# Optimization experiments

Measured on AMD Instinct MI355X. Metric: run time of the kernel, lower is better.

## Reference

```python
import jax, jax.numpy as jnp
import numpy as np


def _skew_relative(QE):
    # QE: [B, H, N, 2N-1] -> [B, H, N, N] relative-position skew (Music-Transformer style)
    B, H, N, L = QE.shape  # L == 2N - 1
    x = jnp.pad(QE, ((0, 0), (0, 0), (0, 0), (0, 1))).reshape(B, H, N * (L + 1))
    x = jnp.pad(x, ((0, 0), (0, 0), (0, N - 1))).reshape(B, H, N + 1, 2 * N - 1)
    return x[:, :, :N, -N:]


def setup_inputs() -> dict:
    key = jax.random.key(0)
    ks = jax.random.split(key, 8)
    B, N, D, H, dh = 8, 1024, 512, 8, 64
    W_SCALE = 0.02
    return {
        "x": jax.random.normal(ks[0], (B, N, D), jnp.float32),
        "phase": jax.random.uniform(ks[1], (B, H, N, 1), jnp.float32),
        "E_rel": jax.random.normal(ks[2], (2 * N - 1, dh), jnp.float32) * 0.05,
        "W_q": jax.random.normal(ks[3], (H * dh, D), jnp.float32) * W_SCALE,
        "W_k": jax.random.normal(ks[4], (H * dh, D), jnp.float32) * W_SCALE,
        "W_v": jax.random.normal(ks[5], (H * dh, D), jnp.float32) * W_SCALE,
        "W_o": jax.random.normal(ks[6], (D, H * dh), jnp.float32) * W_SCALE,
        "b_o": jnp.zeros((D,), jnp.float32),
    }


def reference(x, phase, E_rel, W_q, W_k, W_v, W_o, b_o):
    B, N, _ = x.shape
    H = phase.shape[1]
    dh = W_q.shape[0] // H
    scale = 1.0 / (dh ** 0.5)

    def heads(W):  # [B,N,H*dh] -> [B,H,N,dh]
        return (x @ W.T).reshape(B, N, H, dh).transpose(0, 2, 1, 3)

    Q, K, V = heads(W_q), heads(W_k), heads(W_v)
    attn = jnp.einsum('bhnd,bhmd->bhnm', Q, K)
    attn = attn + _skew_relative(jnp.einsum('bhnd,ld->bhnl', Q, E_rel))
    attn = jax.nn.softmax(attn * scale, axis=-1)
    out = jnp.einsum('bhnm,bhmd->bhnd', attn, V) * phase  # phase-modulated AV
    out = out.transpose(0, 2, 1, 3).reshape(B, N, H * dh)
    return out @ W_o.T + b_o  # dropout is identity in eval mode
```

## Files before the change

### kernel.cpp

```cpp
#include <hip/hip_runtime.h>


typedef __bf16 bf16x8 __attribute__((ext_vector_type(8)));
typedef __bf16 bf16x4 __attribute__((ext_vector_type(4)));
typedef float  f32x4  __attribute__((ext_vector_type(4)));
typedef float  f32x16 __attribute__((ext_vector_type(16)));

#if __has_builtin(__builtin_amdgcn_exp2f)
#define EXP2(x) __builtin_amdgcn_exp2f(x)
#else
#define EXP2(x) exp2f(x)
#endif

#define QSCALE 0.18033688011f

#define GLOAD_LDS16(g, l)                                                      \
    __builtin_amdgcn_global_load_lds(                                          \
        (const __attribute__((address_space(1))) unsigned int*)(g),            \
        (__attribute__((address_space(3))) unsigned int*)(l), 16, 0, 0)


__global__ __launch_bounds__(256) void cvt_all(const float* __restrict__ x,
                                               const float* __restrict__ E,
                                               const float* __restrict__ wq,
                                               const float* __restrict__ wk,
                                               const float* __restrict__ wv,
                                               const float* __restrict__ wo,
                                               __bf16* __restrict__ xb,
                                               __bf16* __restrict__ Ef,
                                               __bf16* __restrict__ wqkv,
                                               __bf16* __restrict__ wob) {
    int i = blockIdx.x * 256 + threadIdx.x;
    if (i >= 1081328 ? i < 1343472 : i < 1048576) {
        const float* s; __bf16* d; int off;
        if      (i < 1048576) { s = x;  d = xb;            off = i; }
        else if (i < 1146864) { s = wq; d = wqkv;          off = i - 1081328; }
        else if (i < 1212400) { s = wk; d = wqkv + 262144; off = i - 1146864; }
        else if (i < 1277936) { s = wv; d = wqkv + 524288; off = i - 1212400; }
        else                  { s = wo; d = wob;           off = i - 1277936; }
        float4 v = *(const float4*)(s + (size_t)off * 4);
        bf16x4 o;
        o[0] = (__bf16)v.x; o[1] = (__bf16)v.y; o[2] = (__bf16)v.z; o[3] = (__bf16)v.w;
        *(bf16x4*)(d + (size_t)off * 4) = o;
    } else if (i >= 1048576 && i < 1081328) {
        int off = i - 1048576;
        float4 v = *(const float4*)(E + (size_t)off * 4);
        int e0i = off * 4;
        int l = e0i >> 6, d0 = e0i & 63;
        int t32 = l >> 5, cq = l & 31, ks = d0 >> 4, hf = (d0 >> 3) & 1, j = d0 & 7;
        bf16x4 o;
        o[0] = (__bf16)v.x; o[1] = (__bf16)v.y; o[2] = (__bf16)v.z; o[3] = (__bf16)v.w;
        *(bf16x4*)(Ef + ((size_t)((t32 * 4 + ks) * 64) + hf * 32 + cq) * 8 + j) = o;
    }
}

__global__ __launch_bounds__(256) void gemm_qkv(const __bf16* __restrict__ X,
                                                const __bf16* __restrict__ W,
                                                __bf16* __restrict__ Qb,
                                                __bf16* __restrict__ Kf,
                                                __bf16* __restrict__ Vf) {
    __shared__ __bf16 Xs[128][64];
    __shared__ __bf16 Ws[128][64];
    const int tid = threadIdx.x;
    const int wave = tid >> 6, lane = tid & 63;
    const int col = lane & 15, quad = lane >> 4;
    const int m_base = blockIdx.x * 128;
    const int j_base = blockIdx.y * 128;
    const bool qk = (j_base < 1024);
    const int wm = (wave & 1) * 64;
    const int wn = (wave >> 1) * 64;
    const f32x4 fz = {0.f, 0.f, 0.f, 0.f};
    f32x4 acc[4][4];
#pragma unroll
    for (int i = 0; i < 4; ++i)
#pragma unroll
        for (int j = 0; j < 4; ++j) acc[i][j] = fz;

    for (int k0 = 0; k0 < 512; k0 += 64) {
#pragma unroll
        for (int p = 0; p < 4; ++p) {
            int s = tid + p * 256;
            int row = s >> 3, cc = (s & 7) * 8;
            GLOAD_LDS16(X + (size_t)(m_base + row) * 512 + k0 + cc, &Xs[0][0] + (size_t)s * 8);
            GLOAD_LDS16(W + (size_t)(j_base + row) * 512 + k0 + cc, &Ws[0][0] + (size_t)s * 8);
        }
        __syncthreads();
#pragma unroll
        for (int kk = 0; kk < 64; kk += 32) {
            bf16x8 xa[4], wb[4];
#pragma unroll
            for (int i = 0; i < 4; ++i) xa[i] = *(const bf16x8*)(&Xs[wm + i * 16 + col][kk + quad * 8]);
#pragma unroll
            for (int j = 0; j < 4; ++j) wb[j] = *(const bf16x8*)(&Ws[wn + j * 16 + col][kk + quad * 8]);
            if (qk) {
#pragma unroll
                for (int i = 0; i < 4; ++i)
#pragma unroll
                    for (int j = 0; j < 4; ++j)
                        acc[i][j] = __builtin_amdgcn_mfma_f32_16x16x32_bf16(wb[i], xa[j], acc[i][j], 0, 0, 0);
            } else {
#pragma unroll
                for (int i = 0; i < 4; ++i)
#pragma unroll
                    for (int j = 0; j < 4; ++j)
                        acc[i][j] = __builtin_amdgcn_mfma_f32_16x16x32_bf16(xa[i], wb[j], acc[i][j], 0, 0, 0);
            }
        }
        __syncthreads();
    }
    if (qk) {
#pragma unroll
        for (int i = 0; i < 4; ++i) {
#pragma unroll
            for (int j = 0; j < 4; ++j) {
                int jabs = j_base + wn + i * 16 + quad * 4;
                int m = m_base + wm + j * 16 + col;
                int b_ = m >> 10, n = m & 1023;
                int rem = jabs & 511, h = rem >> 6, d = rem & 63;
                bf16x4 v;
                if (jabs < 512) {
                    v[0] = (__bf16)(acc[i][j][0] * QSCALE);
                    v[1] = (__bf16)(acc[i][j][1] * QSCALE);
                    v[2] = (__bf16)(acc[i][j][2] * QSCALE);
                    v[3] = (__bf16)(acc[i][j][3] * QSCALE);
                    *(bf16x4*)(Qb + (((size_t)b_ * 8 + h) * 1024 + n) * 64 + d) = v;
                } else {
                    v[0] = (__bf16)acc[i][j][0]; v[1] = (__bf16)acc[i][j][1];
                    v[2] = (__bf16)acc[i][j][2]; v[3] = (__bf16)acc[i][j][3];
                    int t32 = n >> 5, cq = n & 31, ks = d >> 4, hf = (d >> 3) & 1, jj = d & 7;
                    *(bf16x4*)(Kf + (size_t)(b_ * 8 + h) * 65536 +
                               ((size_t)((t32 * 4 + ks) * 64) + hf * 32 + cq) * 8 + jj) = v;
                }
            }
        }
    } else {
#pragma unroll
        for (int i = 0; i < 4; ++i) {
#pragma unroll
            for (int j = 0; j < 4; ++j) {
                int m = m_base + wm + i * 16 + quad * 4;
                int b_ = m >> 10, n = m & 1023;
                int jabs = j_base + wn + j * 16 + col;
                int rem = jabs & 511, h = rem >> 6, d = rem & 63;
                int t64 = n >> 6, ks = (n >> 4) & 3, hf = (n >> 3) & 1, jj = n & 7;
                int dhalf = d >> 5, cq = d & 31;
                bf16x4 v;
                v[0] = (__bf16)acc[i][j][0]; v[1] = (__bf16)acc[i][j][1];
                v[2] = (__bf16)acc[i][j][2]; v[3] = (__bf16)acc[i][j][3];
                *(bf16x4*)(Vf + (size_t)(b_ * 8 + h) * 65536 +
                           ((size_t)(((t64 * 4 + ks) * 2 + dhalf) * 64) + hf * 32 + cq) * 8 + jj) = v;
            }
        }
    }
}

__global__ __launch_bounds__(128, 2) void flash_kernel(const __bf16* __restrict__ Qb,
                                                       const __bf16* __restrict__ Kf,
                                                       const __bf16* __restrict__ Vf,
                                                       const __bf16* __restrict__ Ef,
                                                       const float* __restrict__ phase,
                                                       __bf16* __restrict__ Ob) {
    const int bid = blockIdx.x;
    const int bh = bid & 63;
    const int n0 = (bid >> 6) * 64;
    const int w = threadIdx.x >> 6, lane = threadIdx.x & 63;
    const int colq = lane & 31, half = lane >> 5;
    const int nbase = n0 + w * 32;

    __shared__ __bf16 Pw[2][32][72];

    f32x16 z16;
#pragma unroll
    for (int i = 0; i < 16; ++i) z16[i] = 0.f;

    bf16x8 a_q[4];
#pragma unroll
    for (int ks = 0; ks < 4; ++ks)
        a_q[ks] = *(const bf16x8*)(Qb + ((size_t)bh * 1024 + nbase + colq) * 64 + ks * 16 + half * 8);

    f32x16 o0 = z16, o1 = z16;
    float rowsum[16];
#pragma unroll
    for (int i = 0; i < 16; ++i) rowsum[i] = 0.f;

    const __bf16* Kfb = Kf + (size_t)bh * 65536;
    const __bf16* Vfb = Vf + (size_t)bh * 65536;

#pragma unroll 2
    for (int m0 = 0; m0 < 1024; m0 += 64) {
        const int t32 = m0 >> 5;
        const int te = (m0 - nbase + 992) >> 5;
        f32x16 qe0 = z16, qe1 = z16, qe2 = z16, s0 = z16, s1 = z16;
#pragma unroll
        for (int ks = 0; ks < 4; ++ks) {
            bf16x8 e0 = *(const bf16x8*)(Ef + ((size_t)((te * 4 + ks) * 64) + lane) * 8);
            bf16x8 e1 = *(const bf16x8*)(Ef + ((size_t)(((te + 1) * 4 + ks) * 64) + lane) * 8);
            bf16x8 e2 = *(const bf16x8*)(Ef + ((size_t)(((te + 2) * 4 + ks) * 64) + lane) * 8);
            bf16x8 k0 = *(const bf16x8*)(Kfb + ((size_t)((t32 * 4 + ks) * 64) + lane) * 8);
            bf16x8 k1 = *(const bf16x8*)(Kfb + ((size_t)(((t32 + 1) * 4 + ks) * 64) + lane) * 8);
            qe0 = __builtin_amdgcn_mfma_f32_32x32x16_bf16(a_q[ks], e0, qe0, 0, 0, 0);
            qe1 = __builtin_amdgcn_mfma_f32_32x32x16_bf16(a_q[ks], e1, qe1, 0, 0, 0);
            qe2 = __builtin_amdgcn_mfma_f32_32x32x16_bf16(a_q[ks], e2, qe2, 0, 0, 0);
            s0  = __builtin_amdgcn_mfma_f32_32x32x16_bf16(a_q[ks], k0, s0, 0, 0, 0);
            s1  = __builtin_amdgcn_mfma_f32_32x32x16_bf16(a_q[ks], k1, s1, 0, 0, 0);
        }
#pragma unroll
        for (int r = 0; r < 16; ++r) {
            int row = (r & 3) + 8 * (r >> 2) + 4 * half;
            int tt = colq + 31 - row;
            int src = (tt & 31) | (half << 5);
            float sh0 = __shfl(qe0[r], src, 64);
            float sh1 = __shfl(qe1[r], src, 64);
            float sh2 = __shfl(qe2[r], src, 64);
            bool sel = (tt >= 32);
            float rel0 = sel ? sh1 : sh0;
            float rel1 = sel ? sh2 : sh1;
            float p0 = EXP2(s0[r] + rel0);
            float p1 = EXP2(s1[r] + rel1);
            rowsum[r] += p0 + p1;
            Pw[w][row][colq]      = (__bf16)p0;
            Pw[w][row][32 + colq] = (__bf16)p1;
        }
#pragma unroll
        for (int ks = 0; ks < 4; ++ks) {
            bf16x8 pa = *(const bf16x8*)(&Pw[w][colq][ks * 16 + half * 8]);
            bf16x8 v0 = *(const bf16x8*)(Vfb + ((size_t)((((m0 >> 6) * 4 + ks) * 2 + 0) * 64) + lane) * 8);
            bf16x8 v1 = *(const bf16x8*)(Vfb + ((size_t)((((m0 >> 6) * 4 + ks) * 2 + 1) * 64) + lane) * 8);
            o0 = __builtin_amdgcn_mfma_f32_32x32x16_bf16(pa, v0, o0, 0, 0, 0);
            o1 = __builtin_amdgcn_mfma_f32_32x32x16_bf16(pa, v1, o1, 0, 0, 0);
        }
    }

    const int b_ = bh >> 3, hh = bh & 7;
#pragma unroll
    for (int r = 0; r < 16; ++r) {
        float l = rowsum[r];
        l += __shfl_xor(l, 1, 32);
        l += __shfl_xor(l, 2, 32);
        l += __shfl_xor(l, 4, 32);
        l += __shfl_xor(l, 8, 32);
        l += __shfl_xor(l, 16, 32);
        int row = (r & 3) + 8 * (r >> 2) + 4 * half;
        float f = phase[(size_t)bh * 1024 + nbase + row] / l;
        Pw[w][row][colq]      = (__bf16)(o0[r] * f);
        Pw[w][row][32 + colq] = (__bf16)(o1[r] * f);
    }
    {
        int row = lane >> 1, dseg = lane & 1;
        bf16x8 u0 = *(const bf16x8*)(&Pw[w][row][dseg * 32]);
        bf16x8 u1 = *(const bf16x8*)(&Pw[w][row][dseg * 32 + 8]);
        bf16x8 u2 = *(const bf16x8*)(&Pw[w][row][dseg * 32 + 16]);
        bf16x8 u3 = *(const bf16x8*)(&Pw[w][row][dseg * 32 + 24]);
        size_t obase = ((size_t)b_ * 1024 + nbase + row) * 512 + hh * 64 + dseg * 32;
        *(bf16x8*)(Ob + obase)      = u0;
        *(bf16x8*)(Ob + obase + 8)  = u1;
        *(bf16x8*)(Ob + obase + 16) = u2;
        *(bf16x8*)(Ob + obase + 24) = u3;
    }
}

__global__ __launch_bounds__(256) void gemm_out(const __bf16* __restrict__ X,
                                                const __bf16* __restrict__ W,
                                                const float* __restrict__ bo,
                                                float* __restrict__ out) {
    __shared__ __bf16 Xs[128][64];
    __shared__ __bf16 Ws[128][64];
    const int tid = threadIdx.x;
    const int wave = tid >> 6, lane = tid & 63;
    const int col = lane & 15, quad = lane >> 4;
    const int m_base = blockIdx.x * 128;
    const int j_base = blockIdx.y * 128;
    const int wm = (wave & 1) * 64;
    const int wn = (wave >> 1) * 64;
    const f32x4 fz = {0.f, 0.f, 0.f, 0.f};
    f32x4 acc[4][4];
#pragma unroll
    for (int i = 0; i < 4; ++i)
#pragma unroll
        for (int j = 0; j < 4; ++j) acc[i][j] = fz;

    for (int k0 = 0; k0 < 512; k0 += 64) {
#pragma unroll
        for (int p = 0; p < 4; ++p) {
            int s = tid + p * 256;
            int row = s >> 3, cc = (s & 7) * 8;
            GLOAD_LDS16(X + (size_t)(m_base + row) * 512 + k0 + cc, &Xs[0][0] + (size_t)s * 8);
            GLOAD_LDS16(W + (size_t)(j_base + row) * 512 + k0 + cc, &Ws[0][0] + (size_t)s * 8);
        }
        __syncthreads();
#pragma unroll
        for (int kk = 0; kk < 64; kk += 32) {
            bf16x8 xa[4], wb[4];
#pragma unroll
            for (int i = 0; i < 4; ++i) xa[i] = *(const bf16x8*)(&Xs[wm + i * 16 + col][kk + quad * 8]);
#pragma unroll
            for (int j = 0; j < 4; ++j) wb[j] = *(const bf16x8*)(&Ws[wn + j * 16 + col][kk + quad * 8]);
#pragma unroll
            for (int i = 0; i < 4; ++i)
#pragma unroll
                for (int j = 0; j < 4; ++j)
                    acc[i][j] = __builtin_amdgcn_mfma_f32_16x16x32_bf16(wb[i], xa[j], acc[i][j], 0, 0, 0);
        }
        __syncthreads();
    }
#pragma unroll
    for (int i = 0; i < 4; ++i) {
#pragma unroll
        for (int j = 0; j < 4; ++j) {
            int jabs = j_base + wn + i * 16 + quad * 4;
            int m = m_base + wm + j * 16 + col;
            f32x4 bv = *(const f32x4*)(bo + jabs);
            f32x4 o = acc[i][j] + bv;
            *(f32x4*)(out + (size_t)m * 512 + jabs) = o;
        }
    }
}

extern "C" void kernel_launch(void* const* d_in, const int* in_sizes, int n_in,
                              void* d_out, int out_size, void* d_ws, size_t ws_size,
                              hipStream_t stream) {
    (void)in_sizes; (void)n_in; (void)out_size; (void)ws_size;
    const float* x     = (const float*)d_in[0];
    const float* phase = (const float*)d_in[1];
    const float* E_rel = (const float*)d_in[2];
    const float* W_q   = (const float*)d_in[3];
    const float* W_k   = (const float*)d_in[4];
    const float* W_v   = (const float*)d_in[5];
    const float* W_o   = (const float*)d_in[6];
    const float* b_o   = (const float*)d_in[7];
    float* out = (float*)d_out;

    char* ws = (char*)d_ws;
    __bf16* xb   = (__bf16*)(ws);
    __bf16* wqkv = (__bf16*)(ws + 8388608);
    __bf16* wob  = (__bf16*)(ws + 9961472);
    __bf16* Ef   = (__bf16*)(ws + 10485760);
    __bf16* Qb   = (__bf16*)(ws + 10747904);
    __bf16* Kf   = (__bf16*)(ws + 19136512);
    __bf16* Vf   = (__bf16*)(ws + 27525120);
    __bf16* Ob   = (__bf16*)(ws + 35913728);

    cvt_all<<<dim3(5249), dim3(256), 0, stream>>>(x, E_rel, W_q, W_k, W_v, W_o,
                                                  xb, Ef, wqkv, wob);
    gemm_qkv<<<dim3(64, 12), dim3(256), 0, stream>>>(xb, wqkv, Qb, Kf, Vf);
    flash_kernel<<<dim3(1024), dim3(128), 0, stream>>>(Qb, Kf, Vf, Ef, phase, Ob);
    gemm_out<<<dim3(64, 4), dim3(256), 0, stream>>>(Ob, wob, b_o, out);
}
```

Baseline: 203.3 us.

## Split flash attention over key halves and merge partials in a new kernel

The flash kernel now splits each query tile's key range into two halves, doubling the grid to 2048 blocks. Each block writes unnormalized bf16 partial outputs and row sums to workspace. A new merge kernel adds the two partials, applies phase over the summed denominator, and writes the head-interleaved output. Launch bounds rise to 4 blocks per CU for more occupancy, at the cost of extra global traffic, an extra launch and bf16 rounding of the partials.

```diff
diff --git a/kernel.cpp b/kernel.cpp
--- a/kernel.cpp
+++ b/kernel.cpp
@@ -154,18 +154,20 @@
     }
 }
 
-__global__ __launch_bounds__(128, 2) void flash_kernel(const __bf16* __restrict__ Qb,
+__global__ __launch_bounds__(128, 4) void flash_kernel(const __bf16* __restrict__ Qb,
                                                        const __bf16* __restrict__ Kf,
                                                        const __bf16* __restrict__ Vf,
                                                        const __bf16* __restrict__ Ef,
-                                                       const float* __restrict__ phase,
-                                                       __bf16* __restrict__ Ob) {
+                                                       __bf16* __restrict__ Opart,
+                                                       float* __restrict__ Lpart) {
     const int bid = blockIdx.x;
     const int bh = bid & 63;
-    const int n0 = (bid >> 6) * 64;
+    const int rest = bid >> 6;
+    const int ntile = rest & 15;
+    const int mhalf = rest >> 4;
     const int w = threadIdx.x >> 6, lane = threadIdx.x & 63;
     const int colq = lane & 31, half = lane >> 5;
-    const int nbase = n0 + w * 32;
+    const int nbase = ntile * 64 + w * 32;
 
     __shared__ __bf16 Pw[2][32][72];
 
@@ -187,7 +189,8 @@
     const __bf16* Vfb = Vf + (size_t)bh * 65536;
 
 #pragma unroll 2
-    for (int m0 = 0; m0 < 1024; m0 += 64) {
+    for (int t = 0; t < 8; ++t) {
+        const int m0 = mhalf * 512 + t * 64;
         const int t32 = m0 >> 5;
         const int te = (m0 - nbase + 992) >> 5;
         f32x16 qe0 = z16, qe1 = z16, qe2 = z16, s0 = z16, s1 = z16;
@@ -231,7 +234,6 @@
         }
     }
 
-    const int b_ = bh >> 3, hh = bh & 7;
 #pragma unroll
     for (int r = 0; r < 16; ++r) {
         float l = rowsum[r];
@@ -240,17 +242,63 @@
         l += __shfl_xor(l, 4, 32);
         l += __shfl_xor(l, 8, 32);
         l += __shfl_xor(l, 16, 32);
-        int row = (r & 3) + 8 * (r >> 2) + 4 * half;
-        float f = phase[(size_t)bh * 1024 + nbase + row] / l;
-        Pw[w][row][colq]      = (__bf16)(o0[r] * f);
-        Pw[w][row][32 + colq] = (__bf16)(o1[r] * f);
+        rowsum[r] = l;
+    }
+    if (colq == 0) {
+#pragma unroll
+        for (int r = 0; r < 16; ++r) {
+            int row = (r & 3) + 8 * (r >> 2) + 4 * half;
+            Lpart[(size_t)mhalf * 65536 + (size_t)bh * 1024 + nbase + row] = rowsum[r];
+        }
+    }
+    {
+        const int slot = (bh * 16 + ntile) * 2 + w;
+        __bf16* ob = Opart + ((size_t)mhalf * 2048 + slot) * 2048;
+#pragma unroll
+        for (int rq = 0; rq < 4; ++rq) {
+            bf16x4 c0, c1;
+#pragma unroll
+            for (int i = 0; i < 4; ++i) { c0[i] = (__bf16)o0[rq * 4 + i]; c1[i] = (__bf16)o1[rq * 4 + i]; }
+            *(bf16x4*)(ob + ((size_t)rq * 64 + lane) * 4)       = c0;
+            *(bf16x4*)(ob + ((size_t)(rq + 4) * 64 + lane) * 4) = c1;
+        }
+    }
+}
+
+__global__ __launch_bounds__(256) void merge_kernel(const __bf16* __restrict__ Opart,
+                                                    const float* __restrict__ Lpart,
+                                                    const float* __restrict__ phase,
+                                                    __bf16* __restrict__ Ob) {
+    const int wv = threadIdx.x >> 6, lane = threadIdx.x & 63;
+    const int g = blockIdx.x * 4 + wv;
+    const int w = g & 1, ntile = (g >> 1) & 15, bh = g >> 5;
+    const int nbase = ntile * 64 + w * 32;
+    const int colq = lane & 31, half = lane >> 5;
+
+    __shared__ __bf16 Pw[4][32][72];
+
+    const __bf16* p0 = Opart + (size_t)g * 2048;
+    const __bf16* p1 = Opart + ((size_t)2048 + g) * 2048;
+#pragma unroll
+    for (int rq = 0; rq < 8; ++rq) {
+        bf16x4 a = *(const bf16x4*)(p0 + ((size_t)rq * 64 + lane) * 4);
+        bf16x4 b = *(const bf16x4*)(p1 + ((size_t)rq * 64 + lane) * 4);
+#pragma unroll
+        for (int i = 0; i < 4; ++i) {
+            int row = i + 8 * (rq & 3) + 4 * half;
+            int n = nbase + row;
+            float l = Lpart[(size_t)bh * 1024 + n] + Lpart[65536 + (size_t)bh * 1024 + n];
+            float f = phase[(size_t)bh * 1024 + n] / l;
+            Pw[wv][row][colq + 32 * (rq >> 2)] = (__bf16)(((float)a[i] + (float)b[i]) * f);
+        }
     }
     {
         int row = lane >> 1, dseg = lane & 1;
-        bf16x8 u0 = *(const bf16x8*)(&Pw[w][row][dseg * 32]);
-        bf16x8 u1 = *(const bf16x8*)(&Pw[w][row][dseg * 32 + 8]);
-        bf16x8 u2 = *(const bf16x8*)(&Pw[w][row][dseg * 32 + 16]);
-        bf16x8 u3 = *(const bf16x8*)(&Pw[w][row][dseg * 32 + 24]);
+        int b_ = bh >> 3, hh = bh & 7;
+        bf16x8 u0 = *(const bf16x8*)(&Pw[wv][row][dseg * 32]);
+        bf16x8 u1 = *(const bf16x8*)(&Pw[wv][row][dseg * 32 + 8]);
+        bf16x8 u2 = *(const bf16x8*)(&Pw[wv][row][dseg * 32 + 16]);
+        bf16x8 u3 = *(const bf16x8*)(&Pw[wv][row][dseg * 32 + 24]);
         size_t obase = ((size_t)b_ * 1024 + nbase + row) * 512 + hh * 64 + dseg * 32;
         *(bf16x8*)(Ob + obase)      = u0;
         *(bf16x8*)(Ob + obase + 8)  = u1;
@@ -331,18 +379,21 @@
     float* out = (float*)d_out;
 
     char* ws = (char*)d_ws;
-    __bf16* xb   = (__bf16*)(ws);
-    __bf16* wqkv = (__bf16*)(ws + 8388608);
-    __bf16* wob  = (__bf16*)(ws + 9961472);
-    __bf16* Ef   = (__bf16*)(ws + 10485760);
-    __bf16* Qb   = (__bf16*)(ws + 10747904);
-    __bf16* Kf   = (__bf16*)(ws + 19136512);
-    __bf16* Vf   = (__bf16*)(ws + 27525120);
-    __bf16* Ob   = (__bf16*)(ws + 35913728);
+    __bf16* xb    = (__bf16*)(ws);
+    __bf16* wqkv  = (__bf16*)(ws + 8388608);
+    __bf16* wob   = (__bf16*)(ws + 9961472);
+    __bf16* Ef    = (__bf16*)(ws + 10485760);
+    __bf16* Qb    = (__bf16*)(ws + 10747904);
+    __bf16* Kf    = (__bf16*)(ws + 19136512);
+    __bf16* Vf    = (__bf16*)(ws + 27525120);
+    __bf16* Ob    = (__bf16*)(ws + 35913728);
+    __bf16* Opart = (__bf16*)(ws + 44302336);
+    float*  Lpart = (float*)(ws + 61079552);
 
     cvt_all<<<dim3(5249), dim3(256), 0, stream>>>(x, E_rel, W_q, W_k, W_v, W_o,
                                                   xb, Ef, wqkv, wob);
     gemm_qkv<<<dim3(64, 12), dim3(256), 0, stream>>>(xb, wqkv, Qb, Kf, Vf);
-    flash_kernel<<<dim3(1024), dim3(128), 0, stream>>>(Qb, Kf, Vf, Ef, phase, Ob);
+    flash_kernel<<<dim3(2048), dim3(128), 0, stream>>>(Qb, Kf, Vf, Ef, Opart, Lpart);
+    merge_kernel<<<dim3(512), dim3(256), 0, stream>>>(Opart, Lpart, phase, Ob);
     gemm_out<<<dim3(64, 4), dim3(256), 0, stream>>>(Ob, wob, b_o, out);
 }
```

Measured after the change: 299.5 us. 1.47x slower.

## Reuse relative-position QE tile across iterations and halve gemm_out N-tile

Applied to the files above, without the earlier changes.

The flash kernel now carries the last shifted QE tile in registers from one KV step to the next. That cuts the relative-position MFMAs per 64-key step from three to two and removes one E_rel load stream. The loop is no longer unrolled, and explicit lgkmcnt waits are added around the LDS P buffer. The grid is remapped to 2D so consecutive blocks share the same head, which may improve K/V cache locality. gemm_out uses 64-wide N tiles to launch twice as many blocks, giving better CU coverage at the cost of re-reading X more often.

```diff
diff --git a/kernel.cpp b/kernel.cpp
--- a/kernel.cpp
+++ b/kernel.cpp
@@ -154,15 +154,14 @@
     }
 }
 
-__global__ __launch_bounds__(128, 2) void flash_kernel(const __bf16* __restrict__ Qb,
-                                                       const __bf16* __restrict__ Kf,
-                                                       const __bf16* __restrict__ Vf,
-                                                       const __bf16* __restrict__ Ef,
-                                                       const float* __restrict__ phase,
-                                                       __bf16* __restrict__ Ob) {
-    const int bid = blockIdx.x;
-    const int bh = bid & 63;
-    const int n0 = (bid >> 6) * 64;
+__global__ __launch_bounds__(128) void flash_kernel(const __bf16* __restrict__ Qb,
+                                                    const __bf16* __restrict__ Kf,
+                                                    const __bf16* __restrict__ Vf,
+                                                    const __bf16* __restrict__ Ef,
+                                                    const float* __restrict__ phase,
+                                                    __bf16* __restrict__ Ob) {
+    const int bh = blockIdx.y;
+    const int n0 = blockIdx.x * 64;
     const int w = threadIdx.x >> 6, lane = threadIdx.x & 63;
     const int colq = lane & 31, half = lane >> 5;
     const int nbase = n0 + w * 32;
@@ -186,49 +185,69 @@
     const __bf16* Kfb = Kf + (size_t)bh * 65536;
     const __bf16* Vfb = Vf + (size_t)bh * 65536;
 
-#pragma unroll 2
-    for (int m0 = 0; m0 < 1024; m0 += 64) {
-        const int t32 = m0 >> 5;
-        const int te = (m0 - nbase + 992) >> 5;
-        f32x16 qe0 = z16, qe1 = z16, qe2 = z16, s0 = z16, s1 = z16;
+    const int te0 = (992 - nbase) >> 5;
+
+    float shA[16];
+    {
+        f32x16 qeA = z16;
 #pragma unroll
         for (int ks = 0; ks < 4; ++ks) {
-            bf16x8 e0 = *(const bf16x8*)(Ef + ((size_t)((te * 4 + ks) * 64) + lane) * 8);
-            bf16x8 e1 = *(const bf16x8*)(Ef + ((size_t)(((te + 1) * 4 + ks) * 64) + lane) * 8);
-            bf16x8 e2 = *(const bf16x8*)(Ef + ((size_t)(((te + 2) * 4 + ks) * 64) + lane) * 8);
-            bf16x8 k0 = *(const bf16x8*)(Kfb + ((size_t)((t32 * 4 + ks) * 64) + lane) * 8);
-            bf16x8 k1 = *(const bf16x8*)(Kfb + ((size_t)(((t32 + 1) * 4 + ks) * 64) + lane) * 8);
-            qe0 = __builtin_amdgcn_mfma_f32_32x32x16_bf16(a_q[ks], e0, qe0, 0, 0, 0);
-            qe1 = __builtin_amdgcn_mfma_f32_32x32x16_bf16(a_q[ks], e1, qe1, 0, 0, 0);
-            qe2 = __builtin_amdgcn_mfma_f32_32x32x16_bf16(a_q[ks], e2, qe2, 0, 0, 0);
-            s0  = __builtin_amdgcn_mfma_f32_32x32x16_bf16(a_q[ks], k0, s0, 0, 0, 0);
-            s1  = __builtin_amdgcn_mfma_f32_32x32x16_bf16(a_q[ks], k1, s1, 0, 0, 0);
+            bf16x8 e = *(const bf16x8*)(Ef + ((size_t)((te0 * 4 + ks) * 64) + lane) * 8);
+            qeA = __builtin_amdgcn_mfma_f32_32x32x16_bf16(a_q[ks], e, qeA, 0, 0, 0);
         }
 #pragma unroll
         for (int r = 0; r < 16; ++r) {
             int row = (r & 3) + 8 * (r >> 2) + 4 * half;
             int tt = colq + 31 - row;
             int src = (tt & 31) | (half << 5);
-            float sh0 = __shfl(qe0[r], src, 64);
-            float sh1 = __shfl(qe1[r], src, 64);
-            float sh2 = __shfl(qe2[r], src, 64);
+            shA[r] = __shfl(qeA[r], src, 64);
+        }
+    }
+
+#pragma unroll 1
+    for (int t = 0; t < 16; ++t) {
+        const int m0 = t * 64;
+        const int t32 = m0 >> 5;
+        const int teB = te0 + 2 * t + 1;
+        f32x16 qeB = z16, qeC = z16, s0 = z16, s1 = z16;
+#pragma unroll
+        for (int ks = 0; ks < 4; ++ks) {
+            bf16x8 e1 = *(const bf16x8*)(Ef + ((size_t)((teB * 4 + ks) * 64) + lane) * 8);
+            bf16x8 e2 = *(const bf16x8*)(Ef + ((size_t)(((teB + 1) * 4 + ks) * 64) + lane) * 8);
+            bf16x8 k0 = *(const bf16x8*)(Kfb + ((size_t)((t32 * 4 + ks) * 64) + lane) * 8);
+            bf16x8 k1 = *(const bf16x8*)(Kfb + ((size_t)(((t32 + 1) * 4 + ks) * 64) + lane) * 8);
+            qeB = __builtin_amdgcn_mfma_f32_32x32x16_bf16(a_q[ks], e1, qeB, 0, 0, 0);
+            qeC = __builtin_amdgcn_mfma_f32_32x32x16_bf16(a_q[ks], e2, qeC, 0, 0, 0);
+            s0  = __builtin_amdgcn_mfma_f32_32x32x16_bf16(a_q[ks], k0, s0, 0, 0, 0);
+            s1  = __builtin_amdgcn_mfma_f32_32x32x16_bf16(a_q[ks], k1, s1, 0, 0, 0);
+        }
+#pragma unroll
+        for (int r = 0; r < 16; ++r) {
+            int row = (r & 3) + 8 * (r >> 2) + 4 * half;
+            int tt = colq + 31 - row;
+            int src = (tt & 31) | (half << 5);
+            float shB = __shfl(qeB[r], src, 64);
+            float shC = __shfl(qeC[r], src, 64);
             bool sel = (tt >= 32);
-            float rel0 = sel ? sh1 : sh0;
-            float rel1 = sel ? sh2 : sh1;
+            float rel0 = sel ? shB : shA[r];
+            float rel1 = sel ? shC : shB;
             float p0 = EXP2(s0[r] + rel0);
             float p1 = EXP2(s1[r] + rel1);
             rowsum[r] += p0 + p1;
             Pw[w][row][colq]      = (__bf16)p0;
             Pw[w][row][32 + colq] = (__bf16)p1;
-        }
+            shA[r] = shC;
+        }
+        asm volatile("s_waitcnt lgkmcnt(0)" ::: "memory");
 #pragma unroll
         for (int ks = 0; ks < 4; ++ks) {
             bf16x8 pa = *(const bf16x8*)(&Pw[w][colq][ks * 16 + half * 8]);
-            bf16x8 v0 = *(const bf16x8*)(Vfb + ((size_t)((((m0 >> 6) * 4 + ks) * 2 + 0) * 64) + lane) * 8);
-            bf16x8 v1 = *(const bf16x8*)(Vfb + ((size_t)((((m0 >> 6) * 4 + ks) * 2 + 1) * 64) + lane) * 8);
+            bf16x8 v0 = *(const bf16x8*)(Vfb + ((size_t)(((t * 4 + ks) * 2 + 0) * 64) + lane) * 8);
+            bf16x8 v1 = *(const bf16x8*)(Vfb + ((size_t)(((t * 4 + ks) * 2 + 1) * 64) + lane) * 8);
             o0 = __builtin_amdgcn_mfma_f32_32x32x16_bf16(pa, v0, o0, 0, 0, 0);
             o1 = __builtin_amdgcn_mfma_f32_32x32x16_bf16(pa, v1, o1, 0, 0, 0);
         }
+        asm volatile("" ::: "memory");
     }
 
     const int b_ = bh >> 3, hh = bh & 7;
@@ -245,6 +264,7 @@
         Pw[w][row][colq]      = (__bf16)(o0[r] * f);
         Pw[w][row][32 + colq] = (__bf16)(o1[r] * f);
     }
+    asm volatile("s_waitcnt lgkmcnt(0)" ::: "memory");
     {
         int row = lane >> 1, dseg = lane & 1;
         bf16x8 u0 = *(const bf16x8*)(&Pw[w][row][dseg * 32]);
@@ -264,18 +284,18 @@
                                                 const float* __restrict__ bo,
                                                 float* __restrict__ out) {
     __shared__ __bf16 Xs[128][64];
-    __shared__ __bf16 Ws[128][64];
+    __shared__ __bf16 Ws[64][64];
     const int tid = threadIdx.x;
     const int wave = tid >> 6, lane = tid & 63;
     const int col = lane & 15, quad = lane >> 4;
     const int m_base = blockIdx.x * 128;
-    const int j_base = blockIdx.y * 128;
+    const int j_base = blockIdx.y * 64;
     const int wm = (wave & 1) * 64;
-    const int wn = (wave >> 1) * 64;
+    const int wn = (wave >> 1) * 32;
     const f32x4 fz = {0.f, 0.f, 0.f, 0.f};
-    f32x4 acc[4][4];
-#pragma unroll
-    for (int i = 0; i < 4; ++i)
+    f32x4 acc[2][4];
+#pragma unroll
+    for (int i = 0; i < 2; ++i)
 #pragma unroll
         for (int j = 0; j < 4; ++j) acc[i][j] = fz;
 
@@ -285,18 +305,23 @@
             int s = tid + p * 256;
             int row = s >> 3, cc = (s & 7) * 8;
             GLOAD_LDS16(X + (size_t)(m_base + row) * 512 + k0 + cc, &Xs[0][0] + (size_t)s * 8);
+        }
+#pragma unroll
+        for (int p = 0; p < 2; ++p) {
+            int s = tid + p * 256;
+            int row = s >> 3, cc = (s & 7) * 8;
             GLOAD_LDS16(W + (size_t)(j_base + row) * 512 + k0 + cc, &Ws[0][0] + (size_t)s * 8);
         }
         __syncthreads();
 #pragma unroll
         for (int kk = 0; kk < 64; kk += 32) {
-            bf16x8 xa[4], wb[4];
-#pragma unroll
-            for (int i = 0; i < 4; ++i) xa[i] = *(const bf16x8*)(&Xs[wm + i * 16 + col][kk + quad * 8]);
-#pragma unroll
-            for (int j = 0; j < 4; ++j) wb[j] = *(const bf16x8*)(&Ws[wn + j * 16 + col][kk + quad * 8]);
-#pragma unroll
-            for (int i = 0; i < 4; ++i)
+            bf16x8 xa[4], wb[2];
+#pragma unroll
+            for (int j = 0; j < 4; ++j) xa[j] = *(const bf16x8*)(&Xs[wm + j * 16 + col][kk + quad * 8]);
+#pragma unroll
+            for (int i = 0; i < 2; ++i) wb[i] = *(const bf16x8*)(&Ws[wn + i * 16 + col][kk + quad * 8]);
+#pragma unroll
+            for (int i = 0; i < 2; ++i)
 #pragma unroll
                 for (int j = 0; j < 4; ++j)
                     acc[i][j] = __builtin_amdgcn_mfma_f32_16x16x32_bf16(wb[i], xa[j], acc[i][j], 0, 0, 0);
@@ -304,7 +329,7 @@
         __syncthreads();
     }
 #pragma unroll
-    for (int i = 0; i < 4; ++i) {
+    for (int i = 0; i < 2; ++i) {
 #pragma unroll
         for (int j = 0; j < 4; ++j) {
             int jabs = j_base + wn + i * 16 + quad * 4;
@@ -343,6 +368,6 @@
     cvt_all<<<dim3(5249), dim3(256), 0, stream>>>(x, E_rel, W_q, W_k, W_v, W_o,
                                                   xb, Ef, wqkv, wob);
     gemm_qkv<<<dim3(64, 12), dim3(256), 0, stream>>>(xb, wqkv, Qb, Kf, Vf);
-    flash_kernel<<<dim3(1024), dim3(128), 0, stream>>>(Qb, Kf, Vf, Ef, phase, Ob);
-    gemm_out<<<dim3(64, 4), dim3(256), 0, stream>>>(Ob, wob, b_o, out);
-}
+    flash_kernel<<<dim3(16, 64), dim3(128), 0, stream>>>(Qb, Kf, Vf, Ef, phase, Ob);
+    gemm_out<<<dim3(64, 8), dim3(256), 0, stream>>>(Ob, wob, b_o, out);
+}
```

Result: faster. 183.4 us (-9.8%).
